# Kernel tuning notes

Hardware: AMD Instinct MI355X
Metric: run time of the kernel (lower is better)

Reference implementation:

```python
import jax, jax.numpy as jnp
import numpy as np

DEPTH = 2   # depth
H = 8       # heads
DH = 32     # dim_head
DIM = 256   # model dim (= H*DH)
W = 2       # sliding_window_size
C = 4       # compress_block_size == selection_block_size
NSEL = 2    # num_selected_blocks
B, S = 4, 2048


def layernorm(x, g, b, eps=1e-5):
    m = x.mean(-1, keepdims=True)
    v = jnp.var(x, axis=-1, keepdims=True)
    return (x - m) * jax.lax.rsqrt(v + eps) * g + b


def msoftmax(s, mask):
    # numerically-safe masked softmax; rows with no visible key output zeros
    s = jnp.where(mask, s, -1e9)
    p = jax.nn.softmax(s, axis=-1)
    return jnp.where(jnp.any(mask, axis=-1, keepdims=True), p, 0.0)


def nsa(x, Wq, Wk, Wv, Wg, Wo):
    # Native sparse attention: compressed + top-k selected blocks + sliding window,
    # combined with per-head sigmoid gates.
    b, s, d = x.shape
    nb = s // C
    q = (x @ Wq).reshape(b, s, H, DH).transpose(0, 2, 1, 3)  # [B,H,S,DH]
    k = (x @ Wk).reshape(b, s, H, DH).transpose(0, 2, 1, 3)
    v = (x @ Wv).reshape(b, s, H, DH).transpose(0, 2, 1, 3)
    scale = DH ** -0.5
    t = jnp.arange(s)

    # ---- compressed branch: mean-pooled KV blocks, causal over fully-past blocks
    kb = k.reshape(b, H, nb, C, DH)
    vb = v.reshape(b, H, nb, C, DH)
    kc = kb.mean(3)
    vc = vb.mean(3)
    sc = jnp.einsum('bhsd,bhnd->bhsn', q, kc) * scale       # [B,H,S,nb]
    blk_end = jnp.arange(nb) * C + (C - 1)
    cmask = blk_end[None, :] <= t[:, None]                   # [S,nb]
    pc = msoftmax(sc, cmask[None, None])
    oc = jnp.einsum('bhsn,bhnd->bhsd', pc, vc)

    # ---- selection branch: own block always + top (NSEL-1) blocks by compressed score
    own = t // C                                             # [S]
    not_own = jnp.arange(nb)[None, :] != own[:, None]        # [S,nb]
    sel_scores = jnp.where(not_own[None, None], pc, -1.0)
    top_idx = jax.lax.top_k(sel_scores, NSEL - 1)[1]         # [B,H,S,NSEL-1]
    own_idx = jnp.broadcast_to(own[None, None, :, None], (b, H, s, 1))
    idx = jnp.concatenate([own_idx, top_idx], axis=-1)       # [B,H,S,NSEL]
    idxf = idx.reshape(b, H, s * NSEL, 1, 1)
    sk = jnp.take_along_axis(kb, idxf, axis=2).reshape(b, H, s, NSEL * C, DH)
    sv = jnp.take_along_axis(vb, idxf, axis=2).reshape(b, H, s, NSEL * C, DH)
    pos = (idx[..., None] * C + jnp.arange(C)).reshape(b, H, s, NSEL * C)
    fmask = pos <= t[None, None, :, None]
    sf = jnp.einsum('bhsd,bhskd->bhsk', q, sk) * scale
    pf = msoftmax(sf, fmask)
    of = jnp.einsum('bhsk,bhskd->bhsd', pf, sv)

    # ---- sliding-window branch: causal local window of W tokens (incl. self)
    off = jnp.arange(W) - (W - 1)
    wpos = t[:, None] + off[None, :]                         # [S,W]
    widx = jnp.clip(wpos, 0, s - 1)
    kw = jnp.take(k, widx.reshape(-1), axis=2).reshape(b, H, s, W, DH)
    vw = jnp.take(v, widx.reshape(-1), axis=2).reshape(b, H, s, W, DH)
    sw = jnp.einsum('bhsd,bhsjd->bhsj', q, kw) * scale
    pw = msoftmax(sw, (wpos >= 0)[None, None])
    ow = jnp.einsum('bhsj,bhsjd->bhsd', pw, vw)

    # ---- gated combine + output projection
    g = jax.nn.sigmoid(x @ Wg).reshape(b, s, 3, H).transpose(0, 3, 1, 2)  # [B,H,S,3]
    o = g[..., 0:1] * oc + g[..., 1:2] * of + g[..., 2:3] * ow
    return o.transpose(0, 2, 1, 3).reshape(b, s, H * DH) @ Wo


def forward(x, ln_a_g, ln_a_b, Wq, Wk, Wv, Wg, Wo, ln_f_g, ln_f_b, W1, b1, W2, b2):
    for l in range(DEPTH):
        for j in range(2):  # two attention sub-layers per block
            i = l * 2 + j
            h = layernorm(x, ln_a_g[i], ln_a_b[i])
            x = x + nsa(h, Wq[i], Wk[i], Wv[i], Wg[i], Wo[i])
        h = layernorm(x, ln_f_g[l], ln_f_b[l])
        h = h @ W1[l] + b1[l]
        h = jnp.where(h > 0, h, 0.01 * h)  # LeakyReLU
        x = x + h @ W2[l] + b2[l]
    return x


def setup_inputs() -> dict:
    key = jax.random.key(0)
    ks = jax.random.split(key, 8)
    A = DEPTH * 2
    r = lambda k, shp: jax.random.normal(k, shp, jnp.float32) * 0.02
    return {
        'x': jax.random.normal(ks[0], (B, S, DIM), jnp.float32),
        'ln_a_g': jnp.ones((A, DIM), jnp.float32),
        'ln_a_b': jnp.zeros((A, DIM), jnp.float32),
        'Wq': r(ks[1], (A, DIM, H * DH)),
        'Wk': r(ks[2], (A, DIM, H * DH)),
        'Wv': r(ks[3], (A, DIM, H * DH)),
        'Wg': r(ks[4], (A, DIM, 3 * H)),
        'Wo': r(ks[5], (A, H * DH, DIM)),
        'ln_f_g': jnp.ones((DEPTH, DIM), jnp.float32),
        'ln_f_b': jnp.zeros((DEPTH, DIM), jnp.float32),
        'W1': r(ks[6], (DEPTH, DIM, 2 * DIM)),
        'b1': jnp.zeros((DEPTH, 2 * DIM), jnp.float32),
        'W2': r(ks[7], (DEPTH, 2 * DIM, DIM)),
        'b2': jnp.zeros((DEPTH, DIM), jnp.float32),
    }


def reference(x, ln_a_g, ln_a_b, Wq, Wk, Wv, Wg, Wo, ln_f_g, ln_f_b, W1, b1, W2, b2):
    return forward(x, ln_a_g, ln_a_b, Wq, Wk, Wv, Wg, Wo, ln_f_g, ln_f_b, W1, b1, W2, b2)
```

## Files before the change

kernel.cpp:

```cpp
#include <hip/hip_runtime.h>
#include <hip/hip_bf16.h>
#include <math.h>

#define NH 8
#define DH 32
#define DIM 256
#define SEQ 2048
#define BATCH 4
#define NB 512
#define QKS 512
#define VGS 320
#define SCALE 0.17677669529663687f

typedef short short8v __attribute__((ext_vector_type(8)));
typedef float float4v __attribute__((ext_vector_type(4)));

__device__ __forceinline__ float sigmoidf_(float x){ return 1.f/(1.f+__expf(-x)); }
__device__ __forceinline__ ushort f2bf(float f){
  uint b = __float_as_uint(f);
  return (ushort)((b + 0x7fffu + ((b>>16)&1u)) >> 16);
}
__device__ __forceinline__ float bf2f(ushort u){ return __uint_as_float(((uint)u)<<16); }
__device__ __forceinline__ float bflo(uint u){ return __uint_as_float(u<<16); }
__device__ __forceinline__ float bfhi(uint u){ return __uint_as_float(u & 0xffff0000u); }
__device__ __forceinline__ uint pk2(float a, float b){ return (uint)f2bf(a) | ((uint)f2bf(b)<<16); }
__device__ __forceinline__ void bfu4_to_f32(uint4 u, float* f){
  f[0]=bflo(u.x); f[1]=bfhi(u.x);
  f[2]=bflo(u.y); f[3]=bfhi(u.y);
  f[4]=bflo(u.z); f[5]=bfhi(u.z);
  f[6]=bflo(u.w); f[7]=bfhi(u.w);
}

__global__ void copy_f32(const float* __restrict__ in, float* __restrict__ out, int n4){
  int i = blockIdx.x*blockDim.x + threadIdx.x;
  if (i < n4) ((float4*)out)[i] = ((const float4*)in)[i];
}

__global__ void build_wqk(const float* __restrict__ Wq, const float* __restrict__ Wk, float* __restrict__ out){
  int i = blockIdx.x*256 + threadIdx.x;
  if (i >= 4*256*QKS) return;
  int col = i & 511, rk = (i>>9)&255, l = i>>17;
  out[i] = (col < 256) ? Wq[((size_t)l*256+rk)*256+col] : Wk[((size_t)l*256+rk)*256+col-256];
}
__global__ void build_wvgT(const float* __restrict__ Wv, const float* __restrict__ Wg, ushort* __restrict__ out){
  int i = blockIdx.x*256 + threadIdx.x;
  if (i >= 4*VGS*256) return;
  int k = i & 255, n = (i>>8)%VGS, l = i/(VGS*256);
  float v = 0.f;
  if      (n < 256) v = Wv[((size_t)l*256+k)*256+n];
  else if (n < 280) v = Wg[((size_t)l*256+k)*24 + (n-256)];
  out[i] = f2bf(v);
}
__global__ void build_wT(const float* __restrict__ in, ushort* __restrict__ out, int L, int K, int N){
  int i = blockIdx.x*256 + threadIdx.x;
  if (i >= L*K*N) return;
  int k = i % K, n = (i/K) % N, l = i/(K*N);
  out[i] = f2bf(in[((size_t)l*K+k)*N+n]);
}

__global__ __launch_bounds__(256) void ln_k(const float* __restrict__ x, const float* __restrict__ g,
                                            const float* __restrict__ b, float* __restrict__ h,
                                            ushort* __restrict__ hb){
  int row  = blockIdx.x*4 + (threadIdx.x>>6);
  int lane = threadIdx.x & 63;
  int c = lane*4;
  const float* xr = x + (size_t)row*DIM + c;
  float4 v = *(const float4*)xr;
  float s = v.x+v.y+v.z+v.w;
  float q = v.x*v.x+v.y*v.y+v.z*v.z+v.w*v.w;
  #pragma unroll
  for (int off=32; off>0; off>>=1){ s += __shfl_xor(s, off); q += __shfl_xor(q, off); }
  float mean = s * (1.f/DIM);
  float var  = q * (1.f/DIM) - mean*mean;
  float rs = rsqrtf(var + 1e-5f);
  float4 gg = *(const float4*)(g + c);
  float4 bb = *(const float4*)(b + c);
  float4 o;
  o.x = (v.x-mean)*rs*gg.x + bb.x;
  o.y = (v.y-mean)*rs*gg.y + bb.y;
  o.z = (v.z-mean)*rs*gg.z + bb.z;
  o.w = (v.w-mean)*rs*gg.w + bb.w;
  *(float4*)(h + (size_t)row*DIM + c) = o;
  uint2 u;
  u.x = pk2(o.x, o.y);
  u.y = pk2(o.z, o.w);
  *(uint2*)&hb[(size_t)row*DIM + c] = u;
}

template<bool BIAS, bool LEAKY, bool ACC>
__global__ __launch_bounds__(256) void gemm_f32(const float* __restrict__ A, const float* __restrict__ B,
                                                const float* __restrict__ bias, float* __restrict__ C,
                                                int M, int N, int K){
  __shared__ float As[32][132];
  __shared__ float Bs[32][68];
  int tid = threadIdx.x;
  int m0 = blockIdx.x*128, n0 = blockIdx.y*64;
  int tx = tid & 15, ty = tid >> 4;
  int ar = tid >> 1;
  int ac = (tid & 1)*16;
  int bk = tid >> 3;
  int bn = (tid & 7)*8;
  const float* Ap = A + (size_t)(m0+ar)*K + ac;
  const float* Bp = B + (size_t)bk*N + n0 + bn;
  float4 apre[4], bpre[2];
  #pragma unroll
  for (int j=0;j<4;j++) apre[j] = *(const float4*)(Ap + 4*j);
  bpre[0] = *(const float4*)Bp;
  bpre[1] = *(const float4*)(Bp + 4);
  float acc[8][4];
  #pragma unroll
  for (int i=0;i<8;i++)
    #pragma unroll
    for (int j=0;j<4;j++) acc[i][j]=0.f;
  for (int k0=0; k0<K; k0+=32){
    #pragma unroll
    for (int j=0;j<4;j++){
      As[ac+4*j+0][ar]=apre[j].x; As[ac+4*j+1][ar]=apre[j].y;
      As[ac+4*j+2][ar]=apre[j].z; As[ac+4*j+3][ar]=apre[j].w;
    }
    *(float4*)&Bs[bk][bn]   = bpre[0];
    *(float4*)&Bs[bk][bn+4] = bpre[1];
    __syncthreads();
    if (k0 + 32 < K){
      #pragma unroll
      for (int j=0;j<4;j++) apre[j] = *(const float4*)(Ap + k0 + 32 + 4*j);
      bpre[0] = *(const float4*)(Bp + (size_t)(k0+32)*N);
      bpre[1] = *(const float4*)(Bp + (size_t)(k0+32)*N + 4);
    }
    #pragma unroll
    for (int kk=0;kk<32;kk++){
      float4 bv  = *(const float4*)&Bs[kk][tx*4];
      float4 av0 = *(const float4*)&As[kk][ty*8];
      float4 av1 = *(const float4*)&As[kk][ty*8+4];
      float av[8] = {av0.x,av0.y,av0.z,av0.w,av1.x,av1.y,av1.z,av1.w};
      float bw[4] = {bv.x,bv.y,bv.z,bv.w};
      #pragma unroll
      for (int i=0;i<8;i++)
        #pragma unroll
        for (int j=0;j<4;j++) acc[i][j] += av[i]*bw[j];
    }
    __syncthreads();
  }
  #pragma unroll
  for (int i=0;i<8;i++){
    int m = m0 + ty*8 + i;
    #pragma unroll
    for (int j=0;j<4;j++){
      int n = n0 + tx*4 + j;
      float val = acc[i][j];
      if (BIAS)  val += bias[n];
      if (LEAKY) val = val > 0.f ? val : 0.01f*val;
      float* cp = C + (size_t)m*N + n;
      if (ACC) val += *cp;
      *cp = val;
    }
  }
}

template<bool BIAS, bool LEAKY, bool ACC, bool OBF16>
__global__ __launch_bounds__(256) void gemm_bf16(const ushort* __restrict__ A, const ushort* __restrict__ Bt,
                                                 const float* __restrict__ bias, void* __restrict__ Cv,
                                                 int M, int N, int K){
  __shared__ ushort Al[128*64];
  __shared__ ushort Bl[64*64];
  int tid = threadIdx.x;
  int m0 = blockIdx.x*128, n0 = blockIdx.y*64;
  int w = tid>>6, lane = tid&63;
  int wm = w>>1, wn = w&1;
  float4v acc[4][2];
  #pragma unroll
  for (int i=0;i<4;i++)
    #pragma unroll
    for (int j=0;j<2;j++) acc[i][j] = (float4v){0.f,0.f,0.f,0.f};
  for (int k0=0; k0<K; k0+=64){
    #pragma unroll
    for (int i=0;i<4;i++){
      int id = tid + 256*i;
      int r = id>>3, c = id&7;
      *(uint4*)&Al[r*64 + ((c ^ (r&7))*8)] = *(const uint4*)&A[(size_t)(m0+r)*K + k0 + c*8];
    }
    #pragma unroll
    for (int i=0;i<2;i++){
      int id = tid + 256*i;
      int r = id>>3, c = id&7;
      *(uint4*)&Bl[r*64 + ((c ^ (r&7))*8)] = *(const uint4*)&Bt[(size_t)(n0+r)*K + k0 + c*8];
    }
    __syncthreads();
    #pragma unroll
    for (int kk=0; kk<2; ++kk){
      short8v a[4], bfr[2];
      #pragma unroll
      for (int mf=0; mf<4; mf++){
        int r = wm*64 + mf*16 + (lane&15);
        int c = (kk*4 + (lane>>4)) ^ (r&7);
        a[mf] = *(short8v*)&Al[r*64 + c*8];
      }
      #pragma unroll
      for (int nf=0; nf<2; nf++){
        int r = wn*32 + nf*16 + (lane&15);
        int c = (kk*4 + (lane>>4)) ^ (r&7);
        bfr[nf] = *(short8v*)&Bl[r*64 + c*8];
      }
      #pragma unroll
      for (int mf=0; mf<4; mf++)
        #pragma unroll
        for (int nf=0; nf<2; nf++)
          acc[mf][nf] = __builtin_amdgcn_mfma_f32_16x16x32_bf16(a[mf], bfr[nf], acc[mf][nf], 0, 0, 0);
    }
    __syncthreads();
  }
  #pragma unroll
  for (int nf=0; nf<2; nf++){
    int col = n0 + wn*32 + nf*16 + (lane&15);
    float bv = BIAS ? bias[col] : 0.f;
    #pragma unroll
    for (int mf=0; mf<4; mf++){
      #pragma unroll
      for (int r=0; r<4; r++){
        int row = m0 + wm*64 + mf*16 + (lane>>4)*4 + r;
        float vv = acc[mf][nf][r];
        if (BIAS) vv += bv;
        if (LEAKY) vv = vv > 0.f ? vv : 0.01f*vv;
        if (OBF16) ((ushort*)Cv)[(size_t)row*N + col] = f2bf(vv);
        else {
          float* C = (float*)Cv;
          if (ACC) vv += C[(size_t)row*N + col];
          C[(size_t)row*N + col] = vv;
        }
      }
    }
  }
}

__global__ void pool_k(const float* __restrict__ qk, const ushort* __restrict__ vg,
                       float* __restrict__ kc, ushort* __restrict__ vct){
  int i = blockIdx.x*256 + threadIdx.x;
  if (i >= BATCH*NH*NB*DH) return;
  int d = i & 31, n = (i >> 5) & 511, h = (i >> 14) & 7, b = i >> 17;
  size_t kb = ((size_t)(b*SEQ + n*4))*QKS + 256 + h*DH + d;
  kc[i] = 0.25f*(qk[kb] + qk[kb+QKS] + qk[kb+2*QKS] + qk[kb+3*QKS]);
  size_t vb = ((size_t)(b*SEQ + n*4))*VGS + h*DH + d;
  float pv = 0.25f*(bf2f(vg[vb]) + bf2f(vg[vb+VGS]) + bf2f(vg[vb+2*VGS]) + bf2f(vg[vb+3*VGS]));
  vct[(((size_t)(b*NH + h))*DH + d)*NB + n] = f2bf(pv);
}

__global__ __launch_bounds__(256, 4) void nsa_attn(
    const float* __restrict__ qk, const ushort* __restrict__ vg,
    const float* __restrict__ kc, const ushort* __restrict__ vct,
    ushort* __restrict__ o)
{
  __shared__ float  kt[64*32];
  __shared__ ushort vcT[32*72];
  __shared__ ushort Pl[64*72];
  __shared__ float  ocl[64*36];
  __shared__ float4 meta[4*64];
  int e = blockIdx.x;
  int hh = e & 7;
  int b  = (e >> 3) & 3;
  int qq = (e >> 5) & 7;
  int r  = e >> 8;
  int g  = (r==0) ? (31-qq) : (r==1) ? qq : (r==2) ? (23-qq) : (8+qq);
  int tid = threadIdx.x;
  int w = tid >> 6, lane = tid & 63;
  const float*  kcg  = kc  + ((size_t)(b*NH + hh)*NB)*DH;
  const ushort* vctg = vct + ((size_t)(b*NH + hh)*DH)*NB;

  {
    int t = g*64 + lane;
    int own = t >> 2, nvis = (t+1) >> 2;
    int nmax = 16*(g+1);
    float qv[32];
    {
      const float4* qr = (const float4*)(qk + ((size_t)b*SEQ + t)*QKS + hh*DH);
      #pragma unroll
      for (int d8=0; d8<8; d8++){
        float4 a4 = qr[d8];
        qv[4*d8]=a4.x; qv[4*d8+1]=a4.y; qv[4*d8+2]=a4.z; qv[4*d8+3]=a4.w;
      }
    }
    float l = 0.f, best = -1e30f;
    int bn1 = -1;
    float4v acc0 = (float4v){0.f,0.f,0.f,0.f};
    float4v acc1 = (float4v){0.f,0.f,0.f,0.f};

    int tiles = (g + 4) >> 2;
    for (int ti=0; ti<tiles; ++ti){
      int base = ti*64;
      if (ti) __syncthreads();
      {
        const float4* sk = (const float4*)(kcg + (size_t)base*DH);
        ((float4*)kt)[tid]     = sk[tid];
        ((float4*)kt)[tid+256] = sk[tid+256];
        int sd = tid >> 3, sn = (tid & 7)*8;
        *(uint4*)&vcT[sd*72 + sn] = *(const uint4*)&vctg[(size_t)sd*NB + base + sn];
      }
      __syncthreads();
      float ps[16];
      #pragma unroll
      for (int j=0; j<16; ++j){
        int rr = w*16 + j;
        int n = base + rr;
        float p = 0.f;
        if (n < nmax){
          const float4* kp = (const float4*)&kt[rr*32];
          float s = 0.f;
          #pragma unroll
          for (int d8=0; d8<8; d8++){
            float4 k4 = kp[d8];
            s += qv[4*d8]*k4.x + qv[4*d8+1]*k4.y + qv[4*d8+2]*k4.z + qv[4*d8+3]*k4.w;
          }
          s *= SCALE;
          bool act = (n < nvis);
          if (act && n != own && s > best){ best = s; bn1 = n; }
          p = act ? __expf(s) : 0.f;
          l += p;
        }
        ps[j] = p;
      }
      {
        uint4 u0, u1;
        u0.x = pk2(ps[0],ps[1]);  u0.y = pk2(ps[2],ps[3]);
        u0.z = pk2(ps[4],ps[5]);  u0.w = pk2(ps[6],ps[7]);
        u1.x = pk2(ps[8],ps[9]);  u1.y = pk2(ps[10],ps[11]);
        u1.z = pk2(ps[12],ps[13]);u1.w = pk2(ps[14],ps[15]);
        *(uint4*)&Pl[lane*72 + w*16]     = u0;
        *(uint4*)&Pl[lane*72 + w*16 + 8] = u1;
      }
      __syncthreads();
      #pragma unroll
      for (int ks=0; ks<2; ++ks){
        short8v a  = *(short8v*)&Pl [(16*w + (lane&15))*72 + ks*32 + (lane>>4)*8];
        short8v b0 = *(short8v*)&vcT[(lane&15)*72        + ks*32 + (lane>>4)*8];
        short8v b1 = *(short8v*)&vcT[((lane&15)+16)*72   + ks*32 + (lane>>4)*8];
        acc0 = __builtin_amdgcn_mfma_f32_16x16x32_bf16(a, b0, acc0, 0, 0, 0);
        acc1 = __builtin_amdgcn_mfma_f32_16x16x32_bf16(a, b1, acc1, 0, 0, 0);
      }
    }
    #pragma unroll
    for (int r2=0; r2<4; ++r2){
      int token = 16*w + (lane>>4)*4 + r2;
      ocl[token*36 + (lane&15)]      = acc0[r2];
      ocl[token*36 + 16 + (lane&15)] = acc1[r2];
    }
    meta[w*64 + lane] = make_float4(l, best, __int_as_float(bn1), 0.f);
  }
  __syncthreads();

  {
    int tok = tid >> 2;
    int ds  = (tid & 3)*8;
    int t = g*64 + tok;
    int own = t >> 2, nvis = (t+1) >> 2;
    float q8[8];
    {
      const float4* qr = (const float4*)(qk + ((size_t)b*SEQ + t)*QKS + hh*DH + ds);
      float4 a4 = qr[0], b4 = qr[1];
      q8[0]=a4.x; q8[1]=a4.y; q8[2]=a4.z; q8[3]=a4.w;
      q8[4]=b4.x; q8[5]=b4.y; q8[6]=b4.z; q8[7]=b4.w;
    }
    float out8[8];
    {
      float4 oA = *(const float4*)&ocl[tok*36 + ds];
      float4 oB = *(const float4*)&ocl[tok*36 + ds + 4];
      out8[0]=oA.x; out8[1]=oA.y; out8[2]=oA.z; out8[3]=oA.w;
      out8[4]=oB.x; out8[5]=oB.y; out8[6]=oB.z; out8[7]=oB.w;
    }
    float ll = 0.f, bb = -1e30f;
    int bn = (own==0) ? 1 : 0;
    #pragma unroll
    for (int sp=0; sp<4; ++sp){
      float4 m4 = meta[sp*64 + tok];
      ll += m4.x;
      int mi = __float_as_int(m4.z);
      if (m4.y > bb || (m4.y == bb && mi >= 0 && mi < bn)){ bb = m4.y; bn = mi; }
    }
    const ushort* gr = vg + ((size_t)b*SEQ + t)*VGS + 256;
    float g0 = sigmoidf_(bf2f(gr[hh])), g1 = sigmoidf_(bf2f(gr[8+hh])), g2 = sigmoidf_(bf2f(gr[16+hh]));
    float inv = (nvis > 0) ? g0/ll : 0.f;
    #pragma unroll
    for (int j=0;j<8;j++) out8[j] *= inv;

    const float*  kb2 = qk + (size_t)b*SEQ*QKS + 256 + hh*DH + ds;
    const ushort* vb2 = vg + (size_t)b*SEQ*VGS + hh*DH + ds;
    float s2[8];
    float m2 = -1e30f;
    #pragma unroll
    for (int ki=0; ki<8; ++ki){
      int tt = (ki<4 ? own : bn)*4 + (ki&3);
      float s = -1e30f;
      if (tt <= t){
        const float4* kr = (const float4*)(kb2 + (size_t)tt*QKS);
        float4 a4 = kr[0], c4 = kr[1];
        float ps = q8[0]*a4.x + q8[1]*a4.y + q8[2]*a4.z + q8[3]*a4.w
                 + q8[4]*c4.x + q8[5]*c4.y + q8[6]*c4.z + q8[7]*c4.w;
        ps += __shfl_xor(ps, 1);
        ps += __shfl_xor(ps, 2);
        s = ps*SCALE;
        m2 = fmaxf(m2, s);
      }
      s2[ki] = s;
    }
    float l2 = 0.f;
    #pragma unroll
    for (int ki=0; ki<8; ++ki)
      if (s2[ki] > -1e29f) l2 += __expf(s2[ki] - m2);
    float inv2 = g1/l2;
    #pragma unroll
    for (int ki=0; ki<8; ++ki){
      int tt = (ki<4 ? own : bn)*4 + (ki&3);
      if (tt <= t){
        float pw = __expf(s2[ki] - m2) * inv2;
        uint4 u = *(const uint4*)(vb2 + (size_t)tt*VGS);
        float f[8]; bfu4_to_f32(u, f);
        #pragma unroll
        for (int j=0;j<8;j++) out8[j] += pw*f[j];
      }
    }

    int tp = (t>0) ? t-1 : 0;
    float sa, sb;
    {
      const float4* ka = (const float4*)(kb2 + (size_t)tp*QKS);
      const float4* kb4= (const float4*)(kb2 + (size_t)t *QKS);
      float4 a0 = ka[0], a1 = ka[1], b0 = kb4[0], b1 = kb4[1];
      float pa_ = q8[0]*a0.x + q8[1]*a0.y + q8[2]*a0.z + q8[3]*a0.w
                + q8[4]*a1.x + q8[5]*a1.y + q8[6]*a1.z + q8[7]*a1.w;
      float pb_ = q8[0]*b0.x + q8[1]*b0.y + q8[2]*b0.z + q8[3]*b0.w
                + q8[4]*b1.x + q8[5]*b1.y + q8[6]*b1.z + q8[7]*b1.w;
      pa_ += __shfl_xor(pa_, 1); pa_ += __shfl_xor(pa_, 2);
      pb_ += __shfl_xor(pb_, 1); pb_ += __shfl_xor(pb_, 2);
      sa = pa_*SCALE; sb = pb_*SCALE;
    }
    float m3 = (t>0) ? fmaxf(sa, sb) : sb;
    float pa = (t>0) ? __expf(sa-m3) : 0.f;
    float pb = __expf(sb-m3);
    float inv3 = g2/(pa+pb);
    float va[8], vbv[8];
    bfu4_to_f32(*(const uint4*)(vb2 + (size_t)tp*VGS), va);
    bfu4_to_f32(*(const uint4*)(vb2 + (size_t)t *VGS), vbv);
    ushort* orow = o + ((size_t)b*SEQ + t)*DIM + hh*DH + ds;
    float rr[8];
    #pragma unroll
    for (int j=0;j<8;j++) rr[j] = out8[j] + (pa*va[j] + pb*vbv[j])*inv3;
    uint4 u;
    u.x = pk2(rr[0], rr[1]);
    u.y = pk2(rr[2], rr[3]);
    u.z = pk2(rr[4], rr[5]);
    u.w = pk2(rr[6], rr[7]);
    *(uint4*)orow = u;
  }
}

extern "C" void kernel_launch(void* const* d_in, const int* in_sizes, int n_in,
                              void* d_out, int out_size, void* d_ws, size_t ws_size,
                              hipStream_t stream) {
  const float* x_in   = (const float*)d_in[0];
  const float* ln_a_g = (const float*)d_in[1];
  const float* ln_a_b = (const float*)d_in[2];
  const float* Wq     = (const float*)d_in[3];
  const float* Wk     = (const float*)d_in[4];
  const float* Wv     = (const float*)d_in[5];
  const float* Wg     = (const float*)d_in[6];
  const float* Wo     = (const float*)d_in[7];
  const float* ln_f_g = (const float*)d_in[8];
  const float* ln_f_b = (const float*)d_in[9];
  const float* W1     = (const float*)d_in[10];
  const float* b1     = (const float*)d_in[11];
  const float* W2     = (const float*)d_in[12];
  const float* b2     = (const float*)d_in[13];

  float* xout = (float*)d_out;
  float* ws = (float*)d_ws;
  const size_t NTOK = (size_t)BATCH*SEQ;
  float* h    = ws;
  float* qkb  = h    + NTOK*DIM;
  float* kcb  = qkb  + NTOK*QKS;
  ushort* vctb = (ushort*)(kcb + (size_t)BATCH*NH*NB*DH);
  float* wqk  = (float*)(vctb + (size_t)BATCH*NH*NB*DH);
  ushort* hb   = (ushort*)(wqk + (size_t)4*DIM*QKS);
  ushort* vgu  = hb   + NTOK*DIM;
  ushort* obu  = vgu  + NTOK*VGS;
  ushort* midu = obu  + NTOK*DIM;
  ushort* wvgT = midu + NTOK*512;
  ushort* woT  = wvgT + (size_t)4*VGS*DIM;
  ushort* w1T  = woT  + (size_t)4*DIM*DIM;
  ushort* w2T  = w1T  + (size_t)2*512*DIM;

  copy_f32<<<2048, 256, 0, stream>>>(x_in, xout, (int)(NTOK*DIM/4));
  build_wqk <<<(4*256*QKS+255)/256, 256, 0, stream>>>(Wq, Wk, wqk);
  build_wvgT<<<(4*VGS*256+255)/256, 256, 0, stream>>>(Wv, Wg, wvgT);
  build_wT  <<<(4*256*256+255)/256, 256, 0, stream>>>(Wo, woT, 4, 256, 256);
  build_wT  <<<(2*256*512+255)/256, 256, 0, stream>>>(W1, w1T, 2, 256, 512);
  build_wT  <<<(2*512*256+255)/256, 256, 0, stream>>>(W2, w2T, 2, 512, 256);

  dim3 gqk(64,8), gvg(64,5), g4(64,4), g8(64,8);
  for (int i=0;i<4;i++){
    ln_k<<<2048,256,0,stream>>>(xout, ln_a_g + i*DIM, ln_a_b + i*DIM, h, hb);
    gemm_f32<false,false,false><<<gqk,256,0,stream>>>(h, wqk + (size_t)i*DIM*QKS, nullptr, qkb, 8192,QKS,256);
    gemm_bf16<false,false,false,true><<<gvg,256,0,stream>>>(hb, wvgT + (size_t)i*VGS*DIM, nullptr, vgu, 8192,VGS,256);
    pool_k<<<2048,256,0,stream>>>(qkb, vgu, kcb, vctb);
    nsa_attn<<<1024,256,0,stream>>>(qkb, vgu, kcb, vctb, obu);
    gemm_bf16<false,false,true,false><<<g4,256,0,stream>>>(obu, woT + (size_t)i*DIM*DIM, nullptr, xout, 8192,DIM,256);
    if (i & 1){
      int l = i >> 1;
      ln_k<<<2048,256,0,stream>>>(xout, ln_f_g + l*DIM, ln_f_b + l*DIM, h, hb);
      gemm_bf16<true,true,false,true><<<g8,256,0,stream>>>(hb,   w1T + (size_t)l*512*DIM, b1 + l*512, midu, 8192,512,256);
      gemm_bf16<true,false,true,false><<<g4,256,0,stream>>>(midu, w2T + (size_t)l*DIM*512, b2 + l*DIM, xout, 8192,DIM,512);
    }
  }
}
```

Measured before the change: 543.1 us.

## Split compressed scoring across 8 waves and keep MFMA output in registers

The attention block grows from 256 to 512 threads, so each of 8 waves scores 8 compressed blocks per tile instead of 16, with a trip count bounded by the causal limit. MFMA operands are swapped so the accumulator layout matches the epilogue's token/dim mapping, which drops the ocl shared-memory staging. The epilogue then runs on only 4 waves, with shuffle reductions across lane groups of 16 and 32. This trades more parallel scoring for idle waves in the epilogue and more registers per block under the new launch bounds.

```diff
diff --git a/kernel.cpp b/kernel.cpp
--- a/kernel.cpp
+++ b/kernel.cpp
@@ -29,6 +29,10 @@
   f[2]=bflo(u.y); f[3]=bfhi(u.y);
   f[4]=bflo(u.z); f[5]=bfhi(u.z);
   f[6]=bflo(u.w); f[7]=bfhi(u.w);
+}
+__device__ __forceinline__ void bfu2_to_f32(uint2 u, float* f){
+  f[0]=bflo(u.x); f[1]=bfhi(u.x);
+  f[2]=bflo(u.y); f[3]=bfhi(u.y);
 }
 
 __global__ void copy_f32(const float* __restrict__ in, float* __restrict__ out, int n4){
@@ -244,7 +248,7 @@
   vct[(((size_t)(b*NH + h))*DH + d)*NB + n] = f2bf(pv);
 }
 
-__global__ __launch_bounds__(256, 4) void nsa_attn(
+__global__ __launch_bounds__(512, 6) void nsa_attn(
     const float* __restrict__ qk, const ushort* __restrict__ vg,
     const float* __restrict__ kc, const ushort* __restrict__ vct,
     ushort* __restrict__ o)
@@ -252,8 +256,7 @@
   __shared__ float  kt[64*32];
   __shared__ ushort vcT[32*72];
   __shared__ ushort Pl[64*72];
-  __shared__ float  ocl[64*36];
-  __shared__ float4 meta[4*64];
+  __shared__ float4 meta[8*64];
   int e = blockIdx.x;
   int hh = e & 7;
   int b  = (e >> 3) & 3;
@@ -265,6 +268,9 @@
   const float*  kcg  = kc  + ((size_t)(b*NH + hh)*NB)*DH;
   const ushort* vctg = vct + ((size_t)(b*NH + hh)*DH)*NB;
 
+  float4v acc0 = (float4v){0.f,0.f,0.f,0.f};
+  float4v acc1 = (float4v){0.f,0.f,0.f,0.f};
+
   {
     int t = g*64 + lane;
     int own = t >> 2, nvis = (t+1) >> 2;
@@ -280,8 +286,6 @@
     }
     float l = 0.f, best = -1e30f;
     int bn1 = -1;
-    float4v acc0 = (float4v){0.f,0.f,0.f,0.f};
-    float4v acc1 = (float4v){0.f,0.f,0.f,0.f};
 
     int tiles = (g + 4) >> 2;
     for (int ti=0; ti<tiles; ++ti){
@@ -289,87 +293,79 @@
       if (ti) __syncthreads();
       {
         const float4* sk = (const float4*)(kcg + (size_t)base*DH);
-        ((float4*)kt)[tid]     = sk[tid];
-        ((float4*)kt)[tid+256] = sk[tid+256];
-        int sd = tid >> 3, sn = (tid & 7)*8;
-        *(uint4*)&vcT[sd*72 + sn] = *(const uint4*)&vctg[(size_t)sd*NB + base + sn];
+        ((float4*)kt)[tid] = sk[tid];
+        if (tid < 256){
+          int sd = tid >> 3, sn = (tid & 7)*8;
+          *(uint4*)&vcT[sd*72 + sn] = *(const uint4*)&vctg[(size_t)sd*NB + base + sn];
+        }
       }
       __syncthreads();
-      float ps[16];
-      #pragma unroll
-      for (int j=0; j<16; ++j){
-        int rr = w*16 + j;
+      int jm = nmax - base - 8*w;
+      jm = jm < 0 ? 0 : (jm > 8 ? 8 : jm);
+      float ps[8];
+      #pragma unroll
+      for (int j=0;j<8;j++) ps[j]=0.f;
+      for (int j=0; j<jm; ++j){
+        int rr = 8*w + j;
         int n = base + rr;
-        float p = 0.f;
-        if (n < nmax){
-          const float4* kp = (const float4*)&kt[rr*32];
-          float s = 0.f;
-          #pragma unroll
-          for (int d8=0; d8<8; d8++){
-            float4 k4 = kp[d8];
-            s += qv[4*d8]*k4.x + qv[4*d8+1]*k4.y + qv[4*d8+2]*k4.z + qv[4*d8+3]*k4.w;
-          }
-          s *= SCALE;
-          bool act = (n < nvis);
-          if (act && n != own && s > best){ best = s; bn1 = n; }
-          p = act ? __expf(s) : 0.f;
-          l += p;
+        const float4* kp = (const float4*)&kt[rr*32];
+        float s = 0.f;
+        #pragma unroll
+        for (int d8=0; d8<8; d8++){
+          float4 k4 = kp[d8];
+          s += qv[4*d8]*k4.x + qv[4*d8+1]*k4.y + qv[4*d8+2]*k4.z + qv[4*d8+3]*k4.w;
         }
+        s *= SCALE;
+        bool act = (n < nvis);
+        if (act && n != own && s > best){ best = s; bn1 = n; }
+        float p = act ? __expf(s) : 0.f;
+        l += p;
         ps[j] = p;
       }
       {
-        uint4 u0, u1;
+        uint4 u0;
         u0.x = pk2(ps[0],ps[1]);  u0.y = pk2(ps[2],ps[3]);
         u0.z = pk2(ps[4],ps[5]);  u0.w = pk2(ps[6],ps[7]);
-        u1.x = pk2(ps[8],ps[9]);  u1.y = pk2(ps[10],ps[11]);
-        u1.z = pk2(ps[12],ps[13]);u1.w = pk2(ps[14],ps[15]);
-        *(uint4*)&Pl[lane*72 + w*16]     = u0;
-        *(uint4*)&Pl[lane*72 + w*16 + 8] = u1;
+        *(uint4*)&Pl[lane*72 + w*8] = u0;
       }
       __syncthreads();
-      #pragma unroll
-      for (int ks=0; ks<2; ++ks){
-        short8v a  = *(short8v*)&Pl [(16*w + (lane&15))*72 + ks*32 + (lane>>4)*8];
-        short8v b0 = *(short8v*)&vcT[(lane&15)*72        + ks*32 + (lane>>4)*8];
-        short8v b1 = *(short8v*)&vcT[((lane&15)+16)*72   + ks*32 + (lane>>4)*8];
-        acc0 = __builtin_amdgcn_mfma_f32_16x16x32_bf16(a, b0, acc0, 0, 0, 0);
-        acc1 = __builtin_amdgcn_mfma_f32_16x16x32_bf16(a, b1, acc1, 0, 0, 0);
-      }
-    }
-    #pragma unroll
-    for (int r2=0; r2<4; ++r2){
-      int token = 16*w + (lane>>4)*4 + r2;
-      ocl[token*36 + (lane&15)]      = acc0[r2];
-      ocl[token*36 + 16 + (lane&15)] = acc1[r2];
+      if (w < 4){
+        #pragma unroll
+        for (int ks=0; ks<2; ++ks){
+          short8v bfrag = *(short8v*)&Pl [(16*w + (lane&15))*72 + ks*32 + (lane>>4)*8];
+          short8v a0    = *(short8v*)&vcT[(lane&15)*72          + ks*32 + (lane>>4)*8];
+          short8v a1    = *(short8v*)&vcT[((lane&15)+16)*72     + ks*32 + (lane>>4)*8];
+          acc0 = __builtin_amdgcn_mfma_f32_16x16x32_bf16(a0, bfrag, acc0, 0, 0, 0);
+          acc1 = __builtin_amdgcn_mfma_f32_16x16x32_bf16(a1, bfrag, acc1, 0, 0, 0);
+        }
+      }
     }
     meta[w*64 + lane] = make_float4(l, best, __int_as_float(bn1), 0.f);
   }
   __syncthreads();
 
-  {
-    int tok = tid >> 2;
-    int ds  = (tid & 3)*8;
-    int t = g*64 + tok;
+  if (w < 4){
+    int c = lane & 15, m = lane >> 4;
+    int tokidx = w*16 + c;
+    int t = g*64 + tokidx;
     int own = t >> 2, nvis = (t+1) >> 2;
+    int dA = 4*m, dB = 16 + 4*m;
     float q8[8];
     {
-      const float4* qr = (const float4*)(qk + ((size_t)b*SEQ + t)*QKS + hh*DH + ds);
-      float4 a4 = qr[0], b4 = qr[1];
+      const float* qrow = qk + ((size_t)b*SEQ + t)*QKS + hh*DH;
+      float4 a4 = *(const float4*)(qrow + dA);
+      float4 b4 = *(const float4*)(qrow + dB);
       q8[0]=a4.x; q8[1]=a4.y; q8[2]=a4.z; q8[3]=a4.w;
       q8[4]=b4.x; q8[5]=b4.y; q8[6]=b4.z; q8[7]=b4.w;
     }
     float out8[8];
-    {
-      float4 oA = *(const float4*)&ocl[tok*36 + ds];
-      float4 oB = *(const float4*)&ocl[tok*36 + ds + 4];
-      out8[0]=oA.x; out8[1]=oA.y; out8[2]=oA.z; out8[3]=oA.w;
-      out8[4]=oB.x; out8[5]=oB.y; out8[6]=oB.z; out8[7]=oB.w;
-    }
+    #pragma unroll
+    for (int j=0;j<4;j++){ out8[j] = acc0[j]; out8[4+j] = acc1[j]; }
     float ll = 0.f, bb = -1e30f;
     int bn = (own==0) ? 1 : 0;
     #pragma unroll
-    for (int sp=0; sp<4; ++sp){
-      float4 m4 = meta[sp*64 + tok];
+    for (int sp=0; sp<8; ++sp){
+      float4 m4 = meta[sp*64 + tokidx];
       ll += m4.x;
       int mi = __float_as_int(m4.z);
       if (m4.y > bb || (m4.y == bb && mi >= 0 && mi < bn)){ bb = m4.y; bn = mi; }
@@ -380,8 +376,8 @@
     #pragma unroll
     for (int j=0;j<8;j++) out8[j] *= inv;
 
-    const float*  kb2 = qk + (size_t)b*SEQ*QKS + 256 + hh*DH + ds;
-    const ushort* vb2 = vg + (size_t)b*SEQ*VGS + hh*DH + ds;
+    const float*  kb2 = qk + (size_t)b*SEQ*QKS + 256 + hh*DH;
+    const ushort* vb2 = vg + (size_t)b*SEQ*VGS + hh*DH;
     float s2[8];
     float m2 = -1e30f;
     #pragma unroll
@@ -389,12 +385,13 @@
       int tt = (ki<4 ? own : bn)*4 + (ki&3);
       float s = -1e30f;
       if (tt <= t){
-        const float4* kr = (const float4*)(kb2 + (size_t)tt*QKS);
-        float4 a4 = kr[0], c4 = kr[1];
+        const float* kr = kb2 + (size_t)tt*QKS;
+        float4 a4 = *(const float4*)(kr + dA);
+        float4 c4 = *(const float4*)(kr + dB);
         float ps = q8[0]*a4.x + q8[1]*a4.y + q8[2]*a4.z + q8[3]*a4.w
                  + q8[4]*c4.x + q8[5]*c4.y + q8[6]*c4.z + q8[7]*c4.w;
-        ps += __shfl_xor(ps, 1);
-        ps += __shfl_xor(ps, 2);
+        ps += __shfl_xor(ps, 16);
+        ps += __shfl_xor(ps, 32);
         s = ps*SCALE;
         m2 = fmaxf(m2, s);
       }
@@ -410,44 +407,50 @@
       int tt = (ki<4 ? own : bn)*4 + (ki&3);
       if (tt <= t){
         float pw = __expf(s2[ki] - m2) * inv2;
-        uint4 u = *(const uint4*)(vb2 + (size_t)tt*VGS);
-        float f[8]; bfu4_to_f32(u, f);
+        float fA[4], fB[4];
+        bfu2_to_f32(*(const uint2*)(vb2 + (size_t)tt*VGS + dA), fA);
+        bfu2_to_f32(*(const uint2*)(vb2 + (size_t)tt*VGS + dB), fB);
         #pragma unroll
-        for (int j=0;j<8;j++) out8[j] += pw*f[j];
+        for (int j=0;j<4;j++){ out8[j] += pw*fA[j]; out8[4+j] += pw*fB[j]; }
       }
     }
 
     int tp = (t>0) ? t-1 : 0;
     float sa, sb;
     {
-      const float4* ka = (const float4*)(kb2 + (size_t)tp*QKS);
-      const float4* kb4= (const float4*)(kb2 + (size_t)t *QKS);
-      float4 a0 = ka[0], a1 = ka[1], b0 = kb4[0], b1 = kb4[1];
+      const float* ka = kb2 + (size_t)tp*QKS;
+      const float* kb4= kb2 + (size_t)t *QKS;
+      float4 a0 = *(const float4*)(ka + dA), a1 = *(const float4*)(ka + dB);
+      float4 b0 = *(const float4*)(kb4 + dA), b1 = *(const float4*)(kb4 + dB);
       float pa_ = q8[0]*a0.x + q8[1]*a0.y + q8[2]*a0.z + q8[3]*a0.w
                 + q8[4]*a1.x + q8[5]*a1.y + q8[6]*a1.z + q8[7]*a1.w;
       float pb_ = q8[0]*b0.x + q8[1]*b0.y + q8[2]*b0.z + q8[3]*b0.w
                 + q8[4]*b1.x + q8[5]*b1.y + q8[6]*b1.z + q8[7]*b1.w;
-      pa_ += __shfl_xor(pa_, 1); pa_ += __shfl_xor(pa_, 2);
-      pb_ += __shfl_xor(pb_, 1); pb_ += __shfl_xor(pb_, 2);
+      pa_ += __shfl_xor(pa_, 16); pa_ += __shfl_xor(pa_, 32);
+      pb_ += __shfl_xor(pb_, 16); pb_ += __shfl_xor(pb_, 32);
       sa = pa_*SCALE; sb = pb_*SCALE;
     }
     float m3 = (t>0) ? fmaxf(sa, sb) : sb;
     float pa = (t>0) ? __expf(sa-m3) : 0.f;
     float pb = __expf(sb-m3);
     float inv3 = g2/(pa+pb);
-    float va[8], vbv[8];
-    bfu4_to_f32(*(const uint4*)(vb2 + (size_t)tp*VGS), va);
-    bfu4_to_f32(*(const uint4*)(vb2 + (size_t)t *VGS), vbv);
-    ushort* orow = o + ((size_t)b*SEQ + t)*DIM + hh*DH + ds;
-    float rr[8];
-    #pragma unroll
-    for (int j=0;j<8;j++) rr[j] = out8[j] + (pa*va[j] + pb*vbv[j])*inv3;
-    uint4 u;
-    u.x = pk2(rr[0], rr[1]);
-    u.y = pk2(rr[2], rr[3]);
-    u.z = pk2(rr[4], rr[5]);
-    u.w = pk2(rr[6], rr[7]);
-    *(uint4*)orow = u;
+    float va[4], vaB[4], vbv[4], vbB[4];
+    bfu2_to_f32(*(const uint2*)(vb2 + (size_t)tp*VGS + dA), va);
+    bfu2_to_f32(*(const uint2*)(vb2 + (size_t)tp*VGS + dB), vaB);
+    bfu2_to_f32(*(const uint2*)(vb2 + (size_t)t *VGS + dA), vbv);
+    bfu2_to_f32(*(const uint2*)(vb2 + (size_t)t *VGS + dB), vbB);
+    ushort* orow = o + ((size_t)b*SEQ + t)*DIM + hh*DH;
+    float rrA[4], rrB[4];
+    #pragma unroll
+    for (int j=0;j<4;j++){
+      rrA[j] = out8[j]   + (pa*va[j]  + pb*vbv[j])*inv3;
+      rrB[j] = out8[4+j] + (pa*vaB[j] + pb*vbB[j])*inv3;
+    }
+    uint2 uA, uB;
+    uA.x = pk2(rrA[0], rrA[1]); uA.y = pk2(rrA[2], rrA[3]);
+    uB.x = pk2(rrB[0], rrB[1]); uB.y = pk2(rrB[2], rrB[3]);
+    *(uint2*)&orow[dA] = uA;
+    *(uint2*)&orow[dB] = uB;
   }
 }
 
@@ -499,7 +502,7 @@
     gemm_f32<false,false,false><<<gqk,256,0,stream>>>(h, wqk + (size_t)i*DIM*QKS, nullptr, qkb, 8192,QKS,256);
     gemm_bf16<false,false,false,true><<<gvg,256,0,stream>>>(hb, wvgT + (size_t)i*VGS*DIM, nullptr, vgu, 8192,VGS,256);
     pool_k<<<2048,256,0,stream>>>(qkb, vgu, kcb, vctb);
-    nsa_attn<<<1024,256,0,stream>>>(qkb, vgu, kcb, vctb, obu);
+    nsa_attn<<<1024,512,0,stream>>>(qkb, vgu, kcb, vctb, obu);
     gemm_bf16<false,false,true,false><<<g4,256,0,stream>>>(obu, woT + (size_t)i*DIM*DIM, nullptr, xout, 8192,DIM,256);
     if (i & 1){
       int l = i >> 1;
```

Measured after the change: 604.7 us. 1.11x slower.

## Fuse QK fp32 GEMM, VG bf16 GEMM and block pooling into one kernel

Applied to the files above, without the earlier changes.

Merges the fp32 Q/K projection GEMM and the bf16 V/gate MFMA GEMM into a single launch, dispatching on blockIdx.y, and computes the mean-pooled compressed K and V inside the GEMM epilogues. This removes the separate pool_k kernel and its re-read of qkb and vgu, and cuts two launches per layer down to one. In exchange the two GEMM paths share one shared-memory allocation sized for the larger path, and the epilogues do extra scattered writes into kcb and the transposed vctb layout.

```diff
diff --git a/kernel.cpp b/kernel.cpp
--- a/kernel.cpp
+++ b/kernel.cpp
@@ -87,72 +87,155 @@
   *(uint2*)&hb[(size_t)row*DIM + c] = u;
 }
 
-template<bool BIAS, bool LEAKY, bool ACC>
-__global__ __launch_bounds__(256) void gemm_f32(const float* __restrict__ A, const float* __restrict__ B,
-                                                const float* __restrict__ bias, float* __restrict__ C,
-                                                int M, int N, int K){
-  __shared__ float As[32][132];
-  __shared__ float Bs[32][68];
+__global__ __launch_bounds__(256) void gemm_qkvg(
+    const float* __restrict__ hA, const ushort* __restrict__ hbA,
+    const float* __restrict__ Bqk, const ushort* __restrict__ BvgT,
+    float* __restrict__ qkb, ushort* __restrict__ vgu,
+    float* __restrict__ kcb, ushort* __restrict__ vctb){
+  __shared__ __align__(16) char smem[25600];
   int tid = threadIdx.x;
-  int m0 = blockIdx.x*128, n0 = blockIdx.y*64;
-  int tx = tid & 15, ty = tid >> 4;
-  int ar = tid >> 1;
-  int ac = (tid & 1)*16;
-  int bk = tid >> 3;
-  int bn = (tid & 7)*8;
-  const float* Ap = A + (size_t)(m0+ar)*K + ac;
-  const float* Bp = B + (size_t)bk*N + n0 + bn;
-  float4 apre[4], bpre[2];
-  #pragma unroll
-  for (int j=0;j<4;j++) apre[j] = *(const float4*)(Ap + 4*j);
-  bpre[0] = *(const float4*)Bp;
-  bpre[1] = *(const float4*)(Bp + 4);
-  float acc[8][4];
-  #pragma unroll
-  for (int i=0;i<8;i++)
-    #pragma unroll
-    for (int j=0;j<4;j++) acc[i][j]=0.f;
-  for (int k0=0; k0<K; k0+=32){
-    #pragma unroll
-    for (int j=0;j<4;j++){
-      As[ac+4*j+0][ar]=apre[j].x; As[ac+4*j+1][ar]=apre[j].y;
-      As[ac+4*j+2][ar]=apre[j].z; As[ac+4*j+3][ar]=apre[j].w;
-    }
-    *(float4*)&Bs[bk][bn]   = bpre[0];
-    *(float4*)&Bs[bk][bn+4] = bpre[1];
-    __syncthreads();
-    if (k0 + 32 < K){
-      #pragma unroll
-      for (int j=0;j<4;j++) apre[j] = *(const float4*)(Ap + k0 + 32 + 4*j);
-      bpre[0] = *(const float4*)(Bp + (size_t)(k0+32)*N);
-      bpre[1] = *(const float4*)(Bp + (size_t)(k0+32)*N + 4);
-    }
-    #pragma unroll
-    for (int kk=0;kk<32;kk++){
-      float4 bv  = *(const float4*)&Bs[kk][tx*4];
-      float4 av0 = *(const float4*)&As[kk][ty*8];
-      float4 av1 = *(const float4*)&As[kk][ty*8+4];
-      float av[8] = {av0.x,av0.y,av0.z,av0.w,av1.x,av1.y,av1.z,av1.w};
-      float bw[4] = {bv.x,bv.y,bv.z,bv.w};
-      #pragma unroll
-      for (int i=0;i<8;i++)
-        #pragma unroll
-        for (int j=0;j<4;j++) acc[i][j] += av[i]*bw[j];
-    }
-    __syncthreads();
-  }
-  #pragma unroll
-  for (int i=0;i<8;i++){
-    int m = m0 + ty*8 + i;
-    #pragma unroll
-    for (int j=0;j<4;j++){
-      int n = n0 + tx*4 + j;
-      float val = acc[i][j];
-      if (BIAS)  val += bias[n];
-      if (LEAKY) val = val > 0.f ? val : 0.01f*val;
-      float* cp = C + (size_t)m*N + n;
-      if (ACC) val += *cp;
-      *cp = val;
+  int m0 = blockIdx.x*128;
+  if (blockIdx.y < 8){
+    float (*As)[132] = (float(*)[132])smem;
+    float (*Bs)[68]  = (float(*)[68])(smem + 16896);
+    int n0 = blockIdx.y*64;
+    int tx = tid & 15, tyy = tid >> 4;
+    int ar = tid >> 1;
+    int ac = (tid & 1)*16;
+    int bk = tid >> 3;
+    int bn = (tid & 7)*8;
+    const float* Ap = hA + (size_t)(m0+ar)*256 + ac;
+    const float* Bp = Bqk + (size_t)bk*QKS + n0 + bn;
+    float4 apre[4], bpre[2];
+    #pragma unroll
+    for (int j=0;j<4;j++) apre[j] = *(const float4*)(Ap + 4*j);
+    bpre[0] = *(const float4*)Bp;
+    bpre[1] = *(const float4*)(Bp + 4);
+    float acc[8][4];
+    #pragma unroll
+    for (int i=0;i<8;i++)
+      #pragma unroll
+      for (int j=0;j<4;j++) acc[i][j]=0.f;
+    for (int k0=0; k0<256; k0+=32){
+      #pragma unroll
+      for (int j=0;j<4;j++){
+        As[ac+4*j+0][ar]=apre[j].x; As[ac+4*j+1][ar]=apre[j].y;
+        As[ac+4*j+2][ar]=apre[j].z; As[ac+4*j+3][ar]=apre[j].w;
+      }
+      *(float4*)&Bs[bk][bn]   = bpre[0];
+      *(float4*)&Bs[bk][bn+4] = bpre[1];
+      __syncthreads();
+      if (k0 + 32 < 256){
+        #pragma unroll
+        for (int j=0;j<4;j++) apre[j] = *(const float4*)(Ap + k0 + 32 + 4*j);
+        bpre[0] = *(const float4*)(Bp + (size_t)(k0+32)*QKS);
+        bpre[1] = *(const float4*)(Bp + (size_t)(k0+32)*QKS + 4);
+      }
+      #pragma unroll
+      for (int kk=0;kk<32;kk++){
+        float4 bv  = *(const float4*)&Bs[kk][tx*4];
+        float4 av0 = *(const float4*)&As[kk][tyy*8];
+        float4 av1 = *(const float4*)&As[kk][tyy*8+4];
+        float av[8] = {av0.x,av0.y,av0.z,av0.w,av1.x,av1.y,av1.z,av1.w};
+        float bw[4] = {bv.x,bv.y,bv.z,bv.w};
+        #pragma unroll
+        for (int i=0;i<8;i++)
+          #pragma unroll
+          for (int j=0;j<4;j++) acc[i][j] += av[i]*bw[j];
+      }
+      __syncthreads();
+    }
+    #pragma unroll
+    for (int i=0;i<8;i++){
+      int m = m0 + tyy*8 + i;
+      #pragma unroll
+      for (int j=0;j<4;j++)
+        qkb[(size_t)m*QKS + n0 + tx*4 + j] = acc[i][j];
+    }
+    if (n0 >= 256){
+      #pragma unroll
+      for (int G=0; G<2; ++G){
+        int row = m0 + tyy*8 + 4*G;
+        int bi = row >> 11;
+        int np = (row & 2047) >> 2;
+        #pragma unroll
+        for (int j=0;j<4;j++){
+          int col = n0 + tx*4 + j - 256;
+          int h_ = col >> 5, d = col & 31;
+          float pv = 0.25f*(((acc[4*G][j] + acc[4*G+1][j]) + acc[4*G+2][j]) + acc[4*G+3][j]);
+          kcb[(((size_t)(bi*NH + h_))*NB + np)*DH + d] = pv;
+        }
+      }
+    }
+  } else {
+    ushort* Al = (ushort*)smem;
+    ushort* Bl = (ushort*)(smem + 16384);
+    int n0 = (blockIdx.y - 8)*64;
+    int w = tid>>6, lane = tid&63;
+    int wm = w>>1, wn = w&1;
+    float4v acc[4][2];
+    #pragma unroll
+    for (int i=0;i<4;i++)
+      #pragma unroll
+      for (int j=0;j<2;j++) acc[i][j] = (float4v){0.f,0.f,0.f,0.f};
+    for (int k0=0; k0<256; k0+=64){
+      #pragma unroll
+      for (int i=0;i<4;i++){
+        int id = tid + 256*i;
+        int r = id>>3, c = id&7;
+        *(uint4*)&Al[r*64 + ((c ^ (r&7))*8)] = *(const uint4*)&hbA[(size_t)(m0+r)*256 + k0 + c*8];
+      }
+      #pragma unroll
+      for (int i=0;i<2;i++){
+        int id = tid + 256*i;
+        int r = id>>3, c = id&7;
+        *(uint4*)&Bl[r*64 + ((c ^ (r&7))*8)] = *(const uint4*)&BvgT[(size_t)(n0+r)*256 + k0 + c*8];
+      }
+      __syncthreads();
+      #pragma unroll
+      for (int kk=0; kk<2; ++kk){
+        short8v a[4], bfr[2];
+        #pragma unroll
+        for (int mf=0; mf<4; mf++){
+          int r = wm*64 + mf*16 + (lane&15);
+          int c = (kk*4 + (lane>>4)) ^ (r&7);
+          a[mf] = *(short8v*)&Al[r*64 + c*8];
+        }
+        #pragma unroll
+        for (int nf=0; nf<2; nf++){
+          int r = wn*32 + nf*16 + (lane&15);
+          int c = (kk*4 + (lane>>4)) ^ (r&7);
+          bfr[nf] = *(short8v*)&Bl[r*64 + c*8];
+        }
+        #pragma unroll
+        for (int mf=0; mf<4; mf++)
+          #pragma unroll
+          for (int nf=0; nf<2; nf++)
+            acc[mf][nf] = __builtin_amdgcn_mfma_f32_16x16x32_bf16(a[mf], bfr[nf], acc[mf][nf], 0, 0, 0);
+      }
+      __syncthreads();
+    }
+    #pragma unroll
+    for (int nf=0; nf<2; nf++){
+      int col = n0 + wn*32 + nf*16 + (lane&15);
+      #pragma unroll
+      for (int mf=0; mf<4; mf++){
+        ushort s4[4];
+        #pragma unroll
+        for (int r=0; r<4; r++){
+          int row = m0 + wm*64 + mf*16 + (lane>>4)*4 + r;
+          s4[r] = f2bf(acc[mf][nf][r]);
+          vgu[(size_t)row*VGS + col] = s4[r];
+        }
+        if (col < 256){
+          int row0 = m0 + wm*64 + mf*16 + (lane>>4)*4;
+          int bi = row0 >> 11;
+          int np = (row0 & 2047) >> 2;
+          float pv = 0.25f*(((bf2f(s4[0]) + bf2f(s4[1])) + bf2f(s4[2])) + bf2f(s4[3]));
+          int h_ = col >> 5, d = col & 31;
+          vctb[(((size_t)(bi*NH + h_))*DH + d)*NB + np] = f2bf(pv);
+        }
+      }
     }
   }
 }
@@ -230,18 +313,6 @@
       }
     }
   }
-}
-
-__global__ void pool_k(const float* __restrict__ qk, const ushort* __restrict__ vg,
-                       float* __restrict__ kc, ushort* __restrict__ vct){
-  int i = blockIdx.x*256 + threadIdx.x;
-  if (i >= BATCH*NH*NB*DH) return;
-  int d = i & 31, n = (i >> 5) & 511, h = (i >> 14) & 7, b = i >> 17;
-  size_t kb = ((size_t)(b*SEQ + n*4))*QKS + 256 + h*DH + d;
-  kc[i] = 0.25f*(qk[kb] + qk[kb+QKS] + qk[kb+2*QKS] + qk[kb+3*QKS]);
-  size_t vb = ((size_t)(b*SEQ + n*4))*VGS + h*DH + d;
-  float pv = 0.25f*(bf2f(vg[vb]) + bf2f(vg[vb+VGS]) + bf2f(vg[vb+2*VGS]) + bf2f(vg[vb+3*VGS]));
-  vct[(((size_t)(b*NH + h))*DH + d)*NB + n] = f2bf(pv);
 }
 
 __global__ __launch_bounds__(256, 4) void nsa_attn(
@@ -493,12 +564,11 @@
   build_wT  <<<(2*256*512+255)/256, 256, 0, stream>>>(W1, w1T, 2, 256, 512);
   build_wT  <<<(2*512*256+255)/256, 256, 0, stream>>>(W2, w2T, 2, 512, 256);
 
-  dim3 gqk(64,8), gvg(64,5), g4(64,4), g8(64,8);
+  dim3 gfused(64,13), g4(64,4), g8(64,8);
   for (int i=0;i<4;i++){
     ln_k<<<2048,256,0,stream>>>(xout, ln_a_g + i*DIM, ln_a_b + i*DIM, h, hb);
-    gemm_f32<false,false,false><<<gqk,256,0,stream>>>(h, wqk + (size_t)i*DIM*QKS, nullptr, qkb, 8192,QKS,256);
-    gemm_bf16<false,false,false,true><<<gvg,256,0,stream>>>(hb, wvgT + (size_t)i*VGS*DIM, nullptr, vgu, 8192,VGS,256);
-    pool_k<<<2048,256,0,stream>>>(qkb, vgu, kcb, vctb);
+    gemm_qkvg<<<gfused,256,0,stream>>>(h, hb, wqk + (size_t)i*DIM*QKS, wvgT + (size_t)i*VGS*DIM,
+                                       qkb, vgu, kcb, vctb);
     nsa_attn<<<1024,256,0,stream>>>(qkb, vgu, kcb, vctb, obu);
     gemm_bf16<false,false,true,false><<<g4,256,0,stream>>>(obu, woT + (size_t)i*DIM*DIM, nullptr, xout, 8192,DIM,256);
     if (i & 1){
```

Result: faster. 507.5 us (-6.6%).
